# Kernel tuning notes

Measured on AMD Instinct MI355X. Metric: run time of the kernel, lower is better.

The kernel has to match this reference:

```python
import jax, jax.numpy as jnp
import numpy as np

DIM = 256
CODEBOOK_SIZE = 8192
BATCH, SEQ = 8, 4096


def setup_inputs() -> dict:
    key = jax.random.key(0)
    kx, kc = jax.random.split(key)
    x = jax.random.normal(kx, (BATCH, SEQ, DIM), dtype=jnp.float32)
    codebook = jax.random.normal(kc, (CODEBOOK_SIZE, DIM), dtype=jnp.float32)
    return {"x": x, "codebook": codebook}


def reference(x, codebook):
    # torch.cdist(x, codebook) -> Euclidean distances [B, S, K].
    # argmin over sqrt(d2) == argmin over d2, so compute squared distances
    x_sq = jnp.sum(x * x, axis=-1, keepdims=True)            # [B, S, 1]
    c_sq = jnp.sum(codebook * codebook, axis=-1)             # [K]
    xc = jnp.einsum("bsd,kd->bsk", x, codebook)              # [B, S, K]
    d2 = x_sq - 2.0 * xc + c_sq                              # [B, S, K]
    indices = jnp.argmin(d2, axis=-1)                        # [B, S] int
    quantized = jnp.take(codebook, indices, axis=0)          # [B, S, D]
    return (indices, quantized)
```

## Files before the change

### kernel.cpp

```cpp
#include <hip/hip_runtime.h>
#include <stdint.h>

#define NQ    32768
#define DIM   256
#define KCB   8192

#define T_MARGIN 0.12f
#define XR_CAP   16384
#define LOSCALE     2048.0f
#define INV_LOSCALE (1.0f / 2048.0f)

typedef _Float16 f16;
typedef f16   v8h __attribute__((ext_vector_type(8)));
typedef f16   v4h __attribute__((ext_vector_type(4)));
typedef float v4f __attribute__((ext_vector_type(4)));
typedef const __attribute__((address_space(1))) uint32_t* gas_p;
typedef __attribute__((address_space(3))) uint32_t*       las_p;

#define OFF_CSQ   0
#define OFF_CBT   8192
#define OFF_CBLT  1056768
#define OFF_CNT   2105344
#define OFF_LIST  2105348
#define OFF_CELL  2138118
#define OFF_XR    2203656
#define OFF_PD1   6397960
#define OFF_PD2   6529032
#define OFF_PI1   6660104


__global__ __launch_bounds__(256) void vq_prep(const float* __restrict__ cb,
                                               float* __restrict__ csq,
                                               f16* __restrict__ cbt,
                                               f16* __restrict__ cblt,
                                               int* __restrict__ cnt) {
  if (blockIdx.x == 0 && threadIdx.x == 0) *cnt = 0;
  const int w    = threadIdx.x >> 6;
  const int lane = threadIdx.x & 63;
  const int c    = blockIdx.x * 4 + w;
  float4 v = ((const float4*)(cb + (size_t)c * DIM))[lane];
  float sq = v.x * v.x + v.y * v.y + v.z * v.z + v.w * v.w;
  #pragma unroll
  for (int m = 32; m >= 1; m >>= 1) sq += __shfl_xor(sq, m, 64);
  if (lane == 0) csq[c] = sq;
  if (lane < 32) {
    const int g = lane;
    const float* p = cb + (size_t)c * DIM + g * 8;
    float4 a = *(const float4*)p;
    float4 b = *(const float4*)(p + 4);
    v8h h, l;
    h[0]=(f16)a.x; l[0]=(f16)((a.x-(float)h[0])*LOSCALE);
    h[1]=(f16)a.y; l[1]=(f16)((a.y-(float)h[1])*LOSCALE);
    h[2]=(f16)a.z; l[2]=(f16)((a.z-(float)h[2])*LOSCALE);
    h[3]=(f16)a.w; l[3]=(f16)((a.w-(float)h[3])*LOSCALE);
    h[4]=(f16)b.x; l[4]=(f16)((b.x-(float)h[4])*LOSCALE);
    h[5]=(f16)b.y; l[5]=(f16)((b.y-(float)h[5])*LOSCALE);
    h[6]=(f16)b.z; l[6]=(f16)((b.z-(float)h[6])*LOSCALE);
    h[7]=(f16)b.w; l[7]=(f16)((b.w-(float)h[7])*LOSCALE);
    const int ct = c >> 4, n = c & 15, ks = g >> 2, quad = g & 3;
    const size_t off = ((size_t)(ct * 8 + ks) * 64 + quad * 16 + n) * 8;
    *(v8h*)&cbt[off]  = h;
    *(v8h*)&cblt[off] = l;
  }
}

__global__ __launch_bounds__(256, 2) void vq_stage1(
    const float* __restrict__ x, const float* __restrict__ csq,
    const f16* __restrict__ cbt, float* __restrict__ pd1,
    float* __restrict__ pd2, int* __restrict__ pi1) {
  __shared__ f16 bufs[2][64 * 256];

  const int tid  = threadIdx.x;
  const int lane = tid & 63;
  const int wv   = tid >> 6;
  const int n    = lane & 15;
  const int quad = lane >> 4;
  const int bq   = blockIdx.x >> 2;
  const int cq   = blockIdx.x & 3;
  const int qb   = bq * 128 + wv * 32;
  const int cqb  = cq * 2048;

  auto issue = [&](int ch) {
    const f16* src = cbt + (size_t)(cq * 128 + ch * 4) * 4096;
    f16* dst = &bufs[ch & 1][0];
    #pragma unroll
    for (int i = 0; i < 8; ++i) {
      const int u = wv * 512 + i * 64;
      __builtin_amdgcn_global_load_lds((gas_p)(src + (size_t)(u + lane) * 8),
                                       (las_p)(dst + (size_t)u * 8), 16, 0, 0);
    }
  };

  issue(0);

  v8h af[2][8];
  #pragma unroll
  for (int it = 0; it < 2; ++it) {
    const float* xp = x + (size_t)(qb + it * 16 + n) * DIM + quad * 8;
    #pragma unroll
    for (int ks = 0; ks < 8; ++ks) {
      float4 a = *(const float4*)(xp + ks * 32);
      float4 b = *(const float4*)(xp + ks * 32 + 4);
      v8h t;
      t[0]=(f16)a.x; t[1]=(f16)a.y; t[2]=(f16)a.z; t[3]=(f16)a.w;
      t[4]=(f16)b.x; t[5]=(f16)b.y; t[6]=(f16)b.z; t[7]=(f16)b.w;
      af[it][ks] = t;
    }
  }

  float d1[8], d2[8]; int i1[8];
  #pragma unroll
  for (int s = 0; s < 8; ++s) {
    d1[s] = 3.402823466e38f; d2[s] = 3.402823466e38f; i1[s] = 0;
  }

  for (int ch = 0; ch < 32; ++ch) {
    __syncthreads();
    if (ch + 1 < 32) issue(ch + 1);
    const f16* B = &bufs[ch & 1][0];

    v4f acc[2][4];
    #pragma unroll
    for (int it = 0; it < 2; ++it)
      #pragma unroll
      for (int jt = 0; jt < 4; ++jt) acc[it][jt] = (v4f){0.f, 0.f, 0.f, 0.f};

    #pragma unroll
    for (int ks = 0; ks < 8; ++ks) {
      #pragma unroll
      for (int jt = 0; jt < 4; ++jt) {
        v8h bf = *(const v8h*)&B[(size_t)(jt * 8 + ks) * 512 + lane * 8];
        acc[0][jt] = __builtin_amdgcn_mfma_f32_16x16x32_f16(af[0][ks], bf, acc[0][jt], 0, 0, 0);
        acc[1][jt] = __builtin_amdgcn_mfma_f32_16x16x32_f16(af[1][ks], bf, acc[1][jt], 0, 0, 0);
      }
    }

    const int cb0 = cqb + ch * 64;
    #pragma unroll
    for (int jt = 0; jt < 4; ++jt) {
      const int   cidx = cb0 + jt * 16 + n;
      const float cs2  = csq[cidx];
      #pragma unroll
      for (int it = 0; it < 2; ++it)
        #pragma unroll
        for (int r = 0; r < 4; ++r) {
          const float d = fmaf(acc[it][jt][r], -2.0f, cs2);
          const int s = it * 4 + r;
          const bool lt = d < d1[s];
          d2[s] = fminf(d2[s], fmaxf(d1[s], d));
          i1[s] = lt ? cidx : i1[s];
          d1[s] = fminf(d1[s], d);
        }
    }
  }

  #pragma unroll
  for (int s = 0; s < 8; ++s) {
    float a1 = d1[s], a2 = d2[s];
    int   ai = i1[s];
    #pragma unroll
    for (int m = 1; m <= 8; m <<= 1) {
      float o1 = __shfl_xor(a1, m, 64);
      int   oi = __shfl_xor(ai, m, 64);
      float o2 = __shfl_xor(a2, m, 64);
      bool  lt = (o1 < a1) || (o1 == a1 && oi < ai);
      float l1 = lt ? a1 : o1;
      float w1 = lt ? o1 : a1;
      int   wi = lt ? oi : ai;
      a2 = fminf(l1, fminf(a2, o2));
      a1 = w1; ai = wi;
    }
    if (n == 0) {
      const int q = qb + (s >> 2) * 16 + quad * 4 + (s & 3);
      pd1[cq * NQ + q] = a1;
      pd2[cq * NQ + q] = a2;
      pi1[cq * NQ + q] = ai;
    }
  }
}

__global__ __launch_bounds__(256) void vq_merge(
    const float* __restrict__ pd1, const float* __restrict__ pd2,
    const int* __restrict__ pi1, float* __restrict__ out_idx,
    int* __restrict__ cnt, int* __restrict__ list,
    unsigned long long* __restrict__ cell) {
  const int q = blockIdx.x * 256 + threadIdx.x;
  float a1 = pd1[q], a2 = pd2[q];
  int   ai = pi1[q];
  #pragma unroll
  for (int p = 1; p < 4; ++p) {
    float o1 = pd1[p * NQ + q], o2 = pd2[p * NQ + q];
    int   oi = pi1[p * NQ + q];
    bool  lt = (o1 < a1) || (o1 == a1 && oi < ai);
    float l1 = lt ? a1 : o1;
    float w1 = lt ? o1 : a1;
    int   wi = lt ? oi : ai;
    a2 = fminf(l1, fminf(a2, o2));
    a1 = w1; ai = wi;
  }
  out_idx[q] = (float)ai;
  if (a2 - a1 <= T_MARGIN) {
    int pos = atomicAdd(cnt, 1);
    if (pos < XR_CAP) list[pos] = q;
    cell[q] = 0xFFFFFFFFFFFFFFFFULL;
  }
}

__global__ __launch_bounds__(256) void vq_compact(
    const float* __restrict__ x, const int* __restrict__ cnt,
    const int* __restrict__ list, float* __restrict__ xr) {
  const int m = min(*cnt, XR_CAP);
  const int wv = threadIdx.x >> 6, lane = threadIdx.x & 63;
  for (int i = blockIdx.x * 4 + wv; i < m; i += gridDim.x * 4) {
    const int q = list[i];
    float4 v = ((const float4*)(x + (size_t)q * DIM))[lane];
    ((float4*)(xr + (size_t)i * DIM))[lane] = v;
  }
}

__global__ __launch_bounds__(256) void vq_stage2(
    const float* __restrict__ xr, const float* __restrict__ csq,
    const f16* __restrict__ cbt, const f16* __restrict__ cblt,
    const int* __restrict__ cnt, const int* __restrict__ list,
    unsigned long long* __restrict__ cell) {
  const int count = min(*cnt, XR_CAP);
  const int qt = blockIdx.x >> 2;
  const int cr = blockIdx.x & 3;
  if (qt * 16 >= count) return;
  const int tid = threadIdx.x, lane = tid & 63, wv = tid >> 6;
  const int n = lane & 15, quad = lane >> 4;

  const int qrow = min(qt * 16 + n, count - 1);
  const float* xp = xr + (size_t)qrow * DIM + quad * 8;
  v8h ah[8], al[8];
  #pragma unroll
  for (int ks = 0; ks < 8; ++ks) {
    float4 a = *(const float4*)(xp + ks * 32);
    float4 b = *(const float4*)(xp + ks * 32 + 4);
    v8h h, l;
    h[0]=(f16)a.x; l[0]=(f16)((a.x-(float)h[0])*LOSCALE);
    h[1]=(f16)a.y; l[1]=(f16)((a.y-(float)h[1])*LOSCALE);
    h[2]=(f16)a.z; l[2]=(f16)((a.z-(float)h[2])*LOSCALE);
    h[3]=(f16)a.w; l[3]=(f16)((a.w-(float)h[3])*LOSCALE);
    h[4]=(f16)b.x; l[4]=(f16)((b.x-(float)h[4])*LOSCALE);
    h[5]=(f16)b.y; l[5]=(f16)((b.y-(float)h[5])*LOSCALE);
    h[6]=(f16)b.z; l[6]=(f16)((b.z-(float)h[6])*LOSCALE);
    h[7]=(f16)b.w; l[7]=(f16)((b.w-(float)h[7])*LOSCALE);
    ah[ks] = h; al[ks] = l;
  }

  float bd[4]; int bi[4];
  #pragma unroll
  for (int r = 0; r < 4; ++r) { bd[r] = 3.402823466e38f; bi[r] = 0; }

  const int cbase = cr * 2048;
  for (int ch = 0; ch < 8; ++ch) {
    v4f a1[4], a2[4];
    #pragma unroll
    for (int jt = 0; jt < 4; ++jt) {
      a1[jt] = (v4f){0.f, 0.f, 0.f, 0.f};
      a2[jt] = (v4f){0.f, 0.f, 0.f, 0.f};
    }
    const int ct0 = (cbase + ch * 256 + wv * 64) >> 4;
    #pragma unroll
    for (int ks = 0; ks < 8; ++ks) {
      #pragma unroll
      for (int jt = 0; jt < 4; ++jt) {
        const size_t off = ((size_t)((ct0 + jt) * 8 + ks) * 64 + lane) * 8;
        v8h bh = *(const v8h*)&cbt[off];
        v8h bl = *(const v8h*)&cblt[off];
        a1[jt] = __builtin_amdgcn_mfma_f32_16x16x32_f16(ah[ks], bh, a1[jt], 0, 0, 0);
        a2[jt] = __builtin_amdgcn_mfma_f32_16x16x32_f16(ah[ks], bl, a2[jt], 0, 0, 0);
        a2[jt] = __builtin_amdgcn_mfma_f32_16x16x32_f16(al[ks], bh, a2[jt], 0, 0, 0);
      }
    }
    #pragma unroll
    for (int jt = 0; jt < 4; ++jt) {
      const int c = cbase + ch * 256 + wv * 64 + jt * 16 + n;
      const float cs2 = csq[c];
      #pragma unroll
      for (int r = 0; r < 4; ++r) {
        const float d = cs2 - 2.0f * (a1[jt][r] + a2[jt][r] * INV_LOSCALE);
        if (d < bd[r]) { bd[r] = d; bi[r] = c; }
      }
    }
  }

  __shared__ unsigned long long red[4][16];
  #pragma unroll
  for (int r = 0; r < 4; ++r) {
    unsigned ub = __float_as_uint(bd[r]);
    ub ^= (ub >> 31) ? 0xFFFFFFFFu : 0x80000000u;
    unsigned long long key = ((unsigned long long)ub << 32) | (unsigned)bi[r];
    #pragma unroll
    for (int m = 1; m <= 8; m <<= 1) {
      unsigned long long o = __shfl_xor(key, m, 64);
      if (o < key) key = o;
    }
    if (n == 0) red[wv][quad * 4 + r] = key;
  }
  __syncthreads();
  if (tid < 16) {
    unsigned long long k = red[0][tid];
    #pragma unroll
    for (int w = 1; w < 4; ++w) {
      unsigned long long o = red[w][tid];
      if (o < k) k = o;
    }
    const int q = list[min(qt * 16 + tid, count - 1)];
    atomicMin(&cell[q], k);
  }
}

__global__ __launch_bounds__(256) void vq_fix(const int* __restrict__ cnt,
                                              const int* __restrict__ list,
                                              const unsigned long long* __restrict__ cell,
                                              float* __restrict__ out_idx) {
  const int count = min(*cnt, XR_CAP);
  for (int i = blockIdx.x * 256 + threadIdx.x; i < count; i += gridDim.x * 256) {
    const int q = list[i];
    out_idx[q] = (float)(unsigned)(cell[q] & 0xFFFFFFFFu);
  }
}

__global__ __launch_bounds__(256) void vq_gather(const float* __restrict__ cb,
                                                 const float* __restrict__ idxf,
                                                 float* __restrict__ outq) {
  const int q    = blockIdx.x * 4 + (threadIdx.x >> 6);
  const int lane = threadIdx.x & 63;
  const int idx  = (int)idxf[q];
  float4 v = ((const float4*)(cb + (size_t)idx * DIM))[lane];
  ((float4*)(outq + (size_t)q * DIM))[lane] = v;
}

extern "C" void kernel_launch(void* const* d_in, const int* in_sizes, int n_in,
                              void* d_out, int out_size, void* d_ws, size_t ws_size,
                              hipStream_t stream) {
  const float* x  = (const float*)d_in[0];
  const float* cb = (const float*)d_in[1];
  float* out      = (float*)d_out;

  float* P = out + NQ;
  float* csq  = P + OFF_CSQ;
  f16*   cbt  = (f16*)(P + OFF_CBT);
  f16*   cblt = (f16*)(P + OFF_CBLT);
  int*   cnt  = (int*)(P + OFF_CNT);
  int*   lst  = (int*)(P + OFF_LIST);
  unsigned long long* cel = (unsigned long long*)(P + OFF_CELL);
  float* xr   = P + OFF_XR;
  float* pd1  = P + OFF_PD1;
  float* pd2  = P + OFF_PD2;
  int*   pi1  = (int*)(P + OFF_PI1);
  float* outq = P;

  vq_prep   <<<KCB / 4,  256, 0, stream>>>(cb, csq, cbt, cblt, cnt);
  vq_stage1 <<<1024,     256, 0, stream>>>(x, csq, cbt, pd1, pd2, pi1);
  vq_merge  <<<NQ / 256, 256, 0, stream>>>(pd1, pd2, pi1, out, cnt, lst, cel);
  vq_compact<<<256,      256, 0, stream>>>(x, cnt, lst, xr);
  vq_stage2 <<<(XR_CAP / 16) * 4, 256, 0, stream>>>(xr, csq, cbt, cblt, cnt, lst, cel);
  vq_fix    <<<32,       256, 0, stream>>>(cnt, lst, cel, out);
  vq_gather <<<NQ / 4,   256, 0, stream>>>(cb, out, outq);
}
```

Measured before the change: 323.5 us.

## Enlarge stage1 query tile, drop compact pass, persistent stage2, batch gather

Stage1 now processes 64 queries per wave (4 row tiles) against each LDS codebook chunk, which halves the grid and doubles reuse of each loaded codebook tile. It also loads the codebook norms once per chunk and broadcasts them with shuffles. The compact kernel is removed: stage2 becomes a grid-stride persistent kernel over 256 blocks that reads x through the list indices directly, and the refinement cap is raised to all queries. Prep now uses all lanes to write hi/lo halves, and gather handles four rows per wave. The bigger tile raises register pressure in stage1 and could lower occupancy.

```diff
diff --git a/kernel.cpp b/kernel.cpp
--- a/kernel.cpp
+++ b/kernel.cpp
@@ -6,13 +6,11 @@
 #define KCB   8192
 
 #define T_MARGIN 0.12f
-#define XR_CAP   16384
 #define LOSCALE     2048.0f
 #define INV_LOSCALE (1.0f / 2048.0f)
 
 typedef _Float16 f16;
 typedef f16   v8h __attribute__((ext_vector_type(8)));
-typedef f16   v4h __attribute__((ext_vector_type(4)));
 typedef float v4f __attribute__((ext_vector_type(4)));
 typedef const __attribute__((address_space(1))) uint32_t* gas_p;
 typedef __attribute__((address_space(3))) uint32_t*       las_p;
@@ -22,11 +20,10 @@
 #define OFF_CBLT  1056768
 #define OFF_CNT   2105344
 #define OFF_LIST  2105348
-#define OFF_CELL  2138118
-#define OFF_XR    2203656
-#define OFF_PD1   6397960
-#define OFF_PD2   6529032
-#define OFF_PI1   6660104
+#define OFF_CELL  2138116
+#define OFF_PD1   2269188
+#define OFF_PD2   2400260
+#define OFF_PI1   2531332
 
 
 __global__ __launch_bounds__(256) void vq_prep(const float* __restrict__ cb,
@@ -38,30 +35,28 @@
   const int w    = threadIdx.x >> 6;
   const int lane = threadIdx.x & 63;
   const int c    = blockIdx.x * 4 + w;
-  float4 v = ((const float4*)(cb + (size_t)c * DIM))[lane];
-  float sq = v.x * v.x + v.y * v.y + v.z * v.z + v.w * v.w;
+  float4 vv = ((const float4*)(cb + (size_t)c * DIM))[lane & 63];
+  float sq = vv.x * vv.x + vv.y * vv.y + vv.z * vv.z + vv.w * vv.w;
   #pragma unroll
   for (int m = 32; m >= 1; m >>= 1) sq += __shfl_xor(sq, m, 64);
   if (lane == 0) csq[c] = sq;
-  if (lane < 32) {
-    const int g = lane;
-    const float* p = cb + (size_t)c * DIM + g * 8;
-    float4 a = *(const float4*)p;
-    float4 b = *(const float4*)(p + 4);
-    v8h h, l;
-    h[0]=(f16)a.x; l[0]=(f16)((a.x-(float)h[0])*LOSCALE);
-    h[1]=(f16)a.y; l[1]=(f16)((a.y-(float)h[1])*LOSCALE);
-    h[2]=(f16)a.z; l[2]=(f16)((a.z-(float)h[2])*LOSCALE);
-    h[3]=(f16)a.w; l[3]=(f16)((a.w-(float)h[3])*LOSCALE);
-    h[4]=(f16)b.x; l[4]=(f16)((b.x-(float)h[4])*LOSCALE);
-    h[5]=(f16)b.y; l[5]=(f16)((b.y-(float)h[5])*LOSCALE);
-    h[6]=(f16)b.z; l[6]=(f16)((b.z-(float)h[6])*LOSCALE);
-    h[7]=(f16)b.w; l[7]=(f16)((b.w-(float)h[7])*LOSCALE);
-    const int ct = c >> 4, n = c & 15, ks = g >> 2, quad = g & 3;
-    const size_t off = ((size_t)(ct * 8 + ks) * 64 + quad * 16 + n) * 8;
-    *(v8h*)&cbt[off]  = h;
-    *(v8h*)&cblt[off] = l;
-  }
+  const int g = lane & 31;
+  const float* p = cb + (size_t)c * DIM + g * 8;
+  float4 a = *(const float4*)p;
+  float4 b = *(const float4*)(p + 4);
+  v8h h, l;
+  h[0]=(f16)a.x; l[0]=(f16)((a.x-(float)h[0])*LOSCALE);
+  h[1]=(f16)a.y; l[1]=(f16)((a.y-(float)h[1])*LOSCALE);
+  h[2]=(f16)a.z; l[2]=(f16)((a.z-(float)h[2])*LOSCALE);
+  h[3]=(f16)a.w; l[3]=(f16)((a.w-(float)h[3])*LOSCALE);
+  h[4]=(f16)b.x; l[4]=(f16)((b.x-(float)h[4])*LOSCALE);
+  h[5]=(f16)b.y; l[5]=(f16)((b.y-(float)h[5])*LOSCALE);
+  h[6]=(f16)b.z; l[6]=(f16)((b.z-(float)h[6])*LOSCALE);
+  h[7]=(f16)b.w; l[7]=(f16)((b.w-(float)h[7])*LOSCALE);
+  const int ct = c >> 4, n = c & 15, ks = g >> 2, quad = g & 3;
+  const size_t off = ((size_t)(ct * 8 + ks) * 64 + quad * 16 + n) * 8;
+  if (lane < 32) *(v8h*)&cbt[off]  = h;
+  else           *(v8h*)&cblt[off] = l;
 }
 
 __global__ __launch_bounds__(256, 2) void vq_stage1(
@@ -77,7 +72,7 @@
   const int quad = lane >> 4;
   const int bq   = blockIdx.x >> 2;
   const int cq   = blockIdx.x & 3;
-  const int qb   = bq * 128 + wv * 32;
+  const int qb   = bq * 256 + wv * 64;
   const int cqb  = cq * 2048;
 
   auto issue = [&](int ch) {
@@ -93,9 +88,9 @@
 
   issue(0);
 
-  v8h af[2][8];
-  #pragma unroll
-  for (int it = 0; it < 2; ++it) {
+  v8h af[4][8];
+  #pragma unroll
+  for (int it = 0; it < 4; ++it) {
     const float* xp = x + (size_t)(qb + it * 16 + n) * DIM + quad * 8;
     #pragma unroll
     for (int ks = 0; ks < 8; ++ks) {
@@ -108,9 +103,9 @@
     }
   }
 
-  float d1[8], d2[8]; int i1[8];
-  #pragma unroll
-  for (int s = 0; s < 8; ++s) {
+  float d1[16], d2[16]; int i1[16];
+  #pragma unroll
+  for (int s = 0; s < 16; ++s) {
     d1[s] = 3.402823466e38f; d2[s] = 3.402823466e38f; i1[s] = 0;
   }
 
@@ -118,44 +113,50 @@
     __syncthreads();
     if (ch + 1 < 32) issue(ch + 1);
     const f16* B = &bufs[ch & 1][0];
-
-    v4f acc[2][4];
-    #pragma unroll
-    for (int it = 0; it < 2; ++it)
-      #pragma unroll
-      for (int jt = 0; jt < 4; ++jt) acc[it][jt] = (v4f){0.f, 0.f, 0.f, 0.f};
-
-    #pragma unroll
-    for (int ks = 0; ks < 8; ++ks) {
-      #pragma unroll
-      for (int jt = 0; jt < 4; ++jt) {
-        v8h bf = *(const v8h*)&B[(size_t)(jt * 8 + ks) * 512 + lane * 8];
-        acc[0][jt] = __builtin_amdgcn_mfma_f32_16x16x32_f16(af[0][ks], bf, acc[0][jt], 0, 0, 0);
-        acc[1][jt] = __builtin_amdgcn_mfma_f32_16x16x32_f16(af[1][ks], bf, acc[1][jt], 0, 0, 0);
-      }
-    }
-
     const int cb0 = cqb + ch * 64;
-    #pragma unroll
-    for (int jt = 0; jt < 4; ++jt) {
-      const int   cidx = cb0 + jt * 16 + n;
-      const float cs2  = csq[cidx];
-      #pragma unroll
-      for (int it = 0; it < 2; ++it)
+    const float csqv = csq[cb0 + lane];
+
+    #pragma unroll
+    for (int cc = 0; cc < 2; ++cc) {
+      v4f acc[4][2];
+      #pragma unroll
+      for (int it = 0; it < 4; ++it) {
+        acc[it][0] = (v4f){0.f, 0.f, 0.f, 0.f};
+        acc[it][1] = (v4f){0.f, 0.f, 0.f, 0.f};
+      }
+      #pragma unroll
+      for (int ks = 0; ks < 8; ++ks) {
         #pragma unroll
-        for (int r = 0; r < 4; ++r) {
-          const float d = fmaf(acc[it][jt][r], -2.0f, cs2);
-          const int s = it * 4 + r;
-          const bool lt = d < d1[s];
-          d2[s] = fminf(d2[s], fmaxf(d1[s], d));
-          i1[s] = lt ? cidx : i1[s];
-          d1[s] = fminf(d1[s], d);
+        for (int jt = 0; jt < 2; ++jt) {
+          v8h bf = *(const v8h*)&B[(size_t)((cc * 2 + jt) * 8 + ks) * 512 + lane * 8];
+          #pragma unroll
+          for (int it = 0; it < 4; ++it)
+            acc[it][jt] = __builtin_amdgcn_mfma_f32_16x16x32_f16(
+                af[it][ks], bf, acc[it][jt], 0, 0, 0);
         }
-    }
-  }
-
-  #pragma unroll
-  for (int s = 0; s < 8; ++s) {
+      }
+      #pragma unroll
+      for (int jt = 0; jt < 2; ++jt) {
+        const int  cl   = (cc * 2 + jt) * 16 + n;
+        const int  cidx = cb0 + cl;
+        const float cs2 = __shfl(csqv, cl, 64);
+        #pragma unroll
+        for (int it = 0; it < 4; ++it)
+          #pragma unroll
+          for (int r = 0; r < 4; ++r) {
+            const float d = fmaf(acc[it][jt][r], -2.0f, cs2);
+            const int s = it * 4 + r;
+            const bool lt = d < d1[s];
+            d2[s] = fminf(d2[s], fmaxf(d1[s], d));
+            i1[s] = lt ? cidx : i1[s];
+            d1[s] = fminf(d1[s], d);
+          }
+      }
+    }
+  }
+
+  #pragma unroll
+  for (int s = 0; s < 16; ++s) {
     float a1 = d1[s], a2 = d2[s];
     int   ai = i1[s];
     #pragma unroll
@@ -201,114 +202,107 @@
   out_idx[q] = (float)ai;
   if (a2 - a1 <= T_MARGIN) {
     int pos = atomicAdd(cnt, 1);
-    if (pos < XR_CAP) list[pos] = q;
+    list[pos] = q;
     cell[q] = 0xFFFFFFFFFFFFFFFFULL;
   }
 }
 
-__global__ __launch_bounds__(256) void vq_compact(
-    const float* __restrict__ x, const int* __restrict__ cnt,
-    const int* __restrict__ list, float* __restrict__ xr) {
-  const int m = min(*cnt, XR_CAP);
-  const int wv = threadIdx.x >> 6, lane = threadIdx.x & 63;
-  for (int i = blockIdx.x * 4 + wv; i < m; i += gridDim.x * 4) {
-    const int q = list[i];
-    float4 v = ((const float4*)(x + (size_t)q * DIM))[lane];
-    ((float4*)(xr + (size_t)i * DIM))[lane] = v;
-  }
-}
-
 __global__ __launch_bounds__(256) void vq_stage2(
-    const float* __restrict__ xr, const float* __restrict__ csq,
+    const float* __restrict__ x, const float* __restrict__ csq,
     const f16* __restrict__ cbt, const f16* __restrict__ cblt,
     const int* __restrict__ cnt, const int* __restrict__ list,
     unsigned long long* __restrict__ cell) {
-  const int count = min(*cnt, XR_CAP);
-  const int qt = blockIdx.x >> 2;
-  const int cr = blockIdx.x & 3;
-  if (qt * 16 >= count) return;
+  const int count = min(*cnt, NQ);
+  if (count == 0) return;
+  const int items = ((count + 15) >> 4) * 4;
   const int tid = threadIdx.x, lane = tid & 63, wv = tid >> 6;
   const int n = lane & 15, quad = lane >> 4;
-
-  const int qrow = min(qt * 16 + n, count - 1);
-  const float* xp = xr + (size_t)qrow * DIM + quad * 8;
-  v8h ah[8], al[8];
-  #pragma unroll
-  for (int ks = 0; ks < 8; ++ks) {
-    float4 a = *(const float4*)(xp + ks * 32);
-    float4 b = *(const float4*)(xp + ks * 32 + 4);
-    v8h h, l;
-    h[0]=(f16)a.x; l[0]=(f16)((a.x-(float)h[0])*LOSCALE);
-    h[1]=(f16)a.y; l[1]=(f16)((a.y-(float)h[1])*LOSCALE);
-    h[2]=(f16)a.z; l[2]=(f16)((a.z-(float)h[2])*LOSCALE);
-    h[3]=(f16)a.w; l[3]=(f16)((a.w-(float)h[3])*LOSCALE);
-    h[4]=(f16)b.x; l[4]=(f16)((b.x-(float)h[4])*LOSCALE);
-    h[5]=(f16)b.y; l[5]=(f16)((b.y-(float)h[5])*LOSCALE);
-    h[6]=(f16)b.z; l[6]=(f16)((b.z-(float)h[6])*LOSCALE);
-    h[7]=(f16)b.w; l[7]=(f16)((b.w-(float)h[7])*LOSCALE);
-    ah[ks] = h; al[ks] = l;
-  }
-
-  float bd[4]; int bi[4];
-  #pragma unroll
-  for (int r = 0; r < 4; ++r) { bd[r] = 3.402823466e38f; bi[r] = 0; }
-
-  const int cbase = cr * 2048;
-  for (int ch = 0; ch < 8; ++ch) {
-    v4f a1[4], a2[4];
-    #pragma unroll
-    for (int jt = 0; jt < 4; ++jt) {
-      a1[jt] = (v4f){0.f, 0.f, 0.f, 0.f};
-      a2[jt] = (v4f){0.f, 0.f, 0.f, 0.f};
-    }
-    const int ct0 = (cbase + ch * 256 + wv * 64) >> 4;
+  __shared__ unsigned long long red[4][16];
+
+  for (int item = blockIdx.x; item < items; item += gridDim.x) {
+    const int qt = item >> 2;
+    const int cr = item & 3;
+
+    const int qrow = list[min(qt * 16 + n, count - 1)];
+    const float* xp = x + (size_t)qrow * DIM + quad * 8;
+    v8h ah[8], al[8];
     #pragma unroll
     for (int ks = 0; ks < 8; ++ks) {
+      float4 a = *(const float4*)(xp + ks * 32);
+      float4 b = *(const float4*)(xp + ks * 32 + 4);
+      v8h h, l;
+      h[0]=(f16)a.x; l[0]=(f16)((a.x-(float)h[0])*LOSCALE);
+      h[1]=(f16)a.y; l[1]=(f16)((a.y-(float)h[1])*LOSCALE);
+      h[2]=(f16)a.z; l[2]=(f16)((a.z-(float)h[2])*LOSCALE);
+      h[3]=(f16)a.w; l[3]=(f16)((a.w-(float)h[3])*LOSCALE);
+      h[4]=(f16)b.x; l[4]=(f16)((b.x-(float)h[4])*LOSCALE);
+      h[5]=(f16)b.y; l[5]=(f16)((b.y-(float)h[5])*LOSCALE);
+      h[6]=(f16)b.z; l[6]=(f16)((b.z-(float)h[6])*LOSCALE);
+      h[7]=(f16)b.w; l[7]=(f16)((b.w-(float)h[7])*LOSCALE);
+      ah[ks] = h; al[ks] = l;
+    }
+
+    float bd[4]; int bi[4];
+    #pragma unroll
+    for (int r = 0; r < 4; ++r) { bd[r] = 3.402823466e38f; bi[r] = 0; }
+
+    const int cbase = cr * 2048;
+    for (int ch = 0; ch < 8; ++ch) {
+      v4f a1[4], a2[4];
       #pragma unroll
       for (int jt = 0; jt < 4; ++jt) {
-        const size_t off = ((size_t)((ct0 + jt) * 8 + ks) * 64 + lane) * 8;
-        v8h bh = *(const v8h*)&cbt[off];
-        v8h bl = *(const v8h*)&cblt[off];
-        a1[jt] = __builtin_amdgcn_mfma_f32_16x16x32_f16(ah[ks], bh, a1[jt], 0, 0, 0);
-        a2[jt] = __builtin_amdgcn_mfma_f32_16x16x32_f16(ah[ks], bl, a2[jt], 0, 0, 0);
-        a2[jt] = __builtin_amdgcn_mfma_f32_16x16x32_f16(al[ks], bh, a2[jt], 0, 0, 0);
-      }
-    }
-    #pragma unroll
-    for (int jt = 0; jt < 4; ++jt) {
-      const int c = cbase + ch * 256 + wv * 64 + jt * 16 + n;
-      const float cs2 = csq[c];
-      #pragma unroll
-      for (int r = 0; r < 4; ++r) {
-        const float d = cs2 - 2.0f * (a1[jt][r] + a2[jt][r] * INV_LOSCALE);
-        if (d < bd[r]) { bd[r] = d; bi[r] = c; }
-      }
-    }
-  }
-
-  __shared__ unsigned long long red[4][16];
-  #pragma unroll
-  for (int r = 0; r < 4; ++r) {
-    unsigned ub = __float_as_uint(bd[r]);
-    ub ^= (ub >> 31) ? 0xFFFFFFFFu : 0x80000000u;
-    unsigned long long key = ((unsigned long long)ub << 32) | (unsigned)bi[r];
-    #pragma unroll
-    for (int m = 1; m <= 8; m <<= 1) {
-      unsigned long long o = __shfl_xor(key, m, 64);
-      if (o < key) key = o;
-    }
-    if (n == 0) red[wv][quad * 4 + r] = key;
-  }
-  __syncthreads();
-  if (tid < 16) {
-    unsigned long long k = red[0][tid];
-    #pragma unroll
-    for (int w = 1; w < 4; ++w) {
-      unsigned long long o = red[w][tid];
-      if (o < k) k = o;
-    }
-    const int q = list[min(qt * 16 + tid, count - 1)];
-    atomicMin(&cell[q], k);
+        a1[jt] = (v4f){0.f, 0.f, 0.f, 0.f};
+        a2[jt] = (v4f){0.f, 0.f, 0.f, 0.f};
+      }
+      const int ct0 = (cbase + ch * 256 + wv * 64) >> 4;
+      #pragma unroll
+      for (int ks = 0; ks < 8; ++ks) {
+        #pragma unroll
+        for (int jt = 0; jt < 4; ++jt) {
+          const size_t off = ((size_t)((ct0 + jt) * 8 + ks) * 64 + lane) * 8;
+          v8h bh = *(const v8h*)&cbt[off];
+          v8h bl = *(const v8h*)&cblt[off];
+          a1[jt] = __builtin_amdgcn_mfma_f32_16x16x32_f16(ah[ks], bh, a1[jt], 0, 0, 0);
+          a2[jt] = __builtin_amdgcn_mfma_f32_16x16x32_f16(ah[ks], bl, a2[jt], 0, 0, 0);
+          a2[jt] = __builtin_amdgcn_mfma_f32_16x16x32_f16(al[ks], bh, a2[jt], 0, 0, 0);
+        }
+      }
+      #pragma unroll
+      for (int jt = 0; jt < 4; ++jt) {
+        const int c = cbase + ch * 256 + wv * 64 + jt * 16 + n;
+        const float cs2 = csq[c];
+        #pragma unroll
+        for (int r = 0; r < 4; ++r) {
+          const float d = cs2 - 2.0f * (a1[jt][r] + a2[jt][r] * INV_LOSCALE);
+          if (d < bd[r]) { bd[r] = d; bi[r] = c; }
+        }
+      }
+    }
+
+    #pragma unroll
+    for (int r = 0; r < 4; ++r) {
+      unsigned ub = __float_as_uint(bd[r]);
+      ub ^= (ub >> 31) ? 0xFFFFFFFFu : 0x80000000u;
+      unsigned long long key = ((unsigned long long)ub << 32) | (unsigned)bi[r];
+      #pragma unroll
+      for (int m = 1; m <= 8; m <<= 1) {
+        unsigned long long o = __shfl_xor(key, m, 64);
+        if (o < key) key = o;
+      }
+      if (n == 0) red[wv][quad * 4 + r] = key;
+    }
+    __syncthreads();
+    if (tid < 16) {
+      unsigned long long k = red[0][tid];
+      #pragma unroll
+      for (int w = 1; w < 4; ++w) {
+        unsigned long long o = red[w][tid];
+        if (o < k) k = o;
+      }
+      const int q = list[min(qt * 16 + tid, count - 1)];
+      atomicMin(&cell[q], k);
+    }
+    __syncthreads();
   }
 }
 
@@ -316,7 +310,7 @@
                                               const int* __restrict__ list,
                                               const unsigned long long* __restrict__ cell,
                                               float* __restrict__ out_idx) {
-  const int count = min(*cnt, XR_CAP);
+  const int count = min(*cnt, NQ);
   for (int i = blockIdx.x * 256 + threadIdx.x; i < count; i += gridDim.x * 256) {
     const int q = list[i];
     out_idx[q] = (float)(unsigned)(cell[q] & 0xFFFFFFFFu);
@@ -326,11 +320,15 @@
 __global__ __launch_bounds__(256) void vq_gather(const float* __restrict__ cb,
                                                  const float* __restrict__ idxf,
                                                  float* __restrict__ outq) {
-  const int q    = blockIdx.x * 4 + (threadIdx.x >> 6);
+  const int q0   = blockIdx.x * 16 + (threadIdx.x >> 6) * 4;
   const int lane = threadIdx.x & 63;
-  const int idx  = (int)idxf[q];
-  float4 v = ((const float4*)(cb + (size_t)idx * DIM))[lane];
-  ((float4*)(outq + (size_t)q * DIM))[lane] = v;
+  #pragma unroll
+  for (int k = 0; k < 4; ++k) {
+    const int q   = q0 + k;
+    const int idx = (int)idxf[q];
+    float4 v = ((const float4*)(cb + (size_t)idx * DIM))[lane];
+    ((float4*)(outq + (size_t)q * DIM))[lane] = v;
+  }
 }
 
 extern "C" void kernel_launch(void* const* d_in, const int* in_sizes, int n_in,
@@ -347,17 +345,15 @@
   int*   cnt  = (int*)(P + OFF_CNT);
   int*   lst  = (int*)(P + OFF_LIST);
   unsigned long long* cel = (unsigned long long*)(P + OFF_CELL);
-  float* xr   = P + OFF_XR;
   float* pd1  = P + OFF_PD1;
   float* pd2  = P + OFF_PD2;
   int*   pi1  = (int*)(P + OFF_PI1);
   float* outq = P;
 
-  vq_prep   <<<KCB / 4,  256, 0, stream>>>(cb, csq, cbt, cblt, cnt);
-  vq_stage1 <<<1024,     256, 0, stream>>>(x, csq, cbt, pd1, pd2, pi1);
-  vq_merge  <<<NQ / 256, 256, 0, stream>>>(pd1, pd2, pi1, out, cnt, lst, cel);
-  vq_compact<<<256,      256, 0, stream>>>(x, cnt, lst, xr);
-  vq_stage2 <<<(XR_CAP / 16) * 4, 256, 0, stream>>>(xr, csq, cbt, cblt, cnt, lst, cel);
-  vq_fix    <<<32,       256, 0, stream>>>(cnt, lst, cel, out);
-  vq_gather <<<NQ / 4,   256, 0, stream>>>(cb, out, outq);
-}
+  vq_prep  <<<KCB / 4,  256, 0, stream>>>(cb, csq, cbt, cblt, cnt);
+  vq_stage1<<<512,      256, 0, stream>>>(x, csq, cbt, pd1, pd2, pi1);
+  vq_merge <<<NQ / 256, 256, 0, stream>>>(pd1, pd2, pi1, out, cnt, lst, cel);
+  vq_stage2<<<256,      256, 0, stream>>>(x, csq, cbt, cblt, cnt, lst, cel);
+  vq_fix   <<<32,       256, 0, stream>>>(cnt, lst, cel, out);
+  vq_gather<<<NQ / 16,  256, 0, stream>>>(cb, out, outq);
+}
```

Result: slower. 344.6 us (+6.5%).
